# Kernel optimization log

Hardware: AMD Instinct MI355X
Metric: run time of the kernel (lower is better)

The kernel has to match this reference:

```python
import jax, jax.numpy as jnp
import numpy as np

B, T_ENC, T_DEC, D, H, O = 256, 512, 64, 64, 512, 512


def setup_inputs() -> dict:
    key = jax.random.key(0)
    ks = jax.random.split(key, 13)
    s = 1.0 / np.sqrt(H)  # PyTorch LSTM/Linear init scale
    u = lambda k, shape: jax.random.uniform(k, shape, jnp.float32, -s, s)
    return {
        "enc_inp": jax.random.normal(ks[0], (B, T_ENC, D), jnp.float32),
        "dec_inp": jax.random.normal(ks[1], (B, T_DEC, D), jnp.float32),
        "enc_Wih": u(ks[2], (4 * H, D)),
        "enc_Whh": u(ks[3], (4 * H, H)),
        "enc_bih": u(ks[4], (4 * H,)),
        "enc_bhh": u(ks[5], (4 * H,)),
        "dec_Wih": u(ks[6], (4 * H, D)),
        "dec_Whh": u(ks[7], (4 * H, H)),
        "dec_bih": u(ks[8], (4 * H,)),
        "dec_bhh": u(ks[9], (4 * H,)),
        "out_W": u(ks[10], (O, H)),
        "out_b": u(ks[11], (O,)),
    }


def _lstm_cell(h, c, x_t, Wih, Whh, bih, bhh):
    # PyTorch gate order: i, f, g, o
    z = x_t @ Wih.T + h @ Whh.T + (bih + bhh)  # [B, 4H]
    i, f, g, o = jnp.split(z, 4, axis=-1)
    c2 = jax.nn.sigmoid(f) * c + jax.nn.sigmoid(i) * jnp.tanh(g)
    h2 = jax.nn.sigmoid(o) * jnp.tanh(c2)
    return h2, c2


def reference(enc_inp, dec_inp, enc_Wih, enc_Whh, enc_bih, enc_bhh,
              dec_Wih, dec_Whh, dec_bih, dec_bhh, out_W, out_b):
    b = enc_inp.shape[0]
    h0 = jnp.zeros((b, H), enc_inp.dtype)
    c0 = jnp.zeros((b, H), enc_inp.dtype)

    # Encoder: single-layer LSTM over T_enc; only final (h, c) are used.
    def enc_step(carry, x_t):
        h, c = carry
        h2, c2 = _lstm_cell(h, c, x_t, enc_Wih, enc_Whh, enc_bih, enc_bhh)
        return (h2, c2), None

    (h, c), _ = jax.lax.scan(enc_step, (h0, c0), jnp.swapaxes(enc_inp, 0, 1))

    # Decoder: fused per-step LSTM + output projection over T_dec.
    def dec_step(carry, x_t):
        h, c = carry
        h2, c2 = _lstm_cell(h, c, x_t, dec_Wih, dec_Whh, dec_bih, dec_bhh)
        y = h2 @ out_W.T + out_b
        return (h2, c2), (y, h2)

    _, (ys, hs) = jax.lax.scan(dec_step, (h, c), jnp.swapaxes(dec_inp, 0, 1))

    dec_outputs = jnp.swapaxes(ys, 0, 1)  # [B, T_dec, O]
    dec_hiddens = jnp.swapaxes(hs, 0, 1)  # [B, T_dec, H]
    return dec_outputs, dec_hiddens
```

## Files before the change

### kernel.cpp

```cpp
#include <hip/hip_runtime.h>

typedef unsigned short ushort_t;
typedef unsigned long long u64;
typedef __attribute__((ext_vector_type(8))) __bf16 bf16x8;
typedef __attribute__((ext_vector_type(4))) float f32x4;

#define B 256
#define TENC 512
#define TDEC 64
#define DIN 64
#define HD 512
#define OD 512
#define GG 256
#define NGRP 16
#define KTOT 576
#define KI 18
#define NT 512

__device__ __forceinline__ float b2f(ushort_t v) {
  union { unsigned u; float f; } x; x.u = ((unsigned)v) << 16; return x.f;
}
__device__ __forceinline__ ushort_t f2b(float f) {
  union { float f; unsigned u; } x; x.f = f;
  unsigned r = x.u + 0x7fffu + ((x.u >> 16) & 1u);
  return (ushort_t)(r >> 16);
}
__device__ __forceinline__ float sigmf(float x) { return 1.f / (1.f + __expf(-x)); }
__device__ __forceinline__ float tanhf_fast(float x) {
  float e = __expf(2.f * x);
  return 1.f - 2.f / (e + 1.f);
}
__device__ __forceinline__ float ld_elem(const void* p, size_t i, bool f32) {
  return f32 ? ((const float*)p)[i] : b2f(((const ushort_t*)p)[i]);
}
__device__ __forceinline__ bf16x8 cvt8(const float* f) {
  f32x4 u = *(const f32x4*)f, v = *(const f32x4*)(f + 4);
  bf16x8 r;
  r[0] = (__bf16)u[0]; r[1] = (__bf16)u[1]; r[2] = (__bf16)u[2]; r[3] = (__bf16)u[3];
  r[4] = (__bf16)v[0]; r[5] = (__bf16)v[1]; r[6] = (__bf16)v[2]; r[7] = (__bf16)v[3];
  return r;
}
__device__ __forceinline__ bf16x8 ld_h16(const ushort_t* p) {
  union { u64 q[2]; bf16x8 v; } x;
  x.q[0] = __hip_atomic_load((const u64*)p,     __ATOMIC_RELAXED, __HIP_MEMORY_SCOPE_AGENT);
  x.q[1] = __hip_atomic_load((const u64*)p + 1, __ATOMIC_RELAXED, __HIP_MEMORY_SCOPE_AGENT);
  return x.v;
}

__global__ void detect(const ushort_t* w, unsigned* flag) {
  if (threadIdx.x == 0) {
    unsigned f = 0;
    for (int i = 0; i < 128; ++i) {
      float v = b2f(w[i]);
      if (!(v * v < 1.f)) f = 1;
    }
    *flag = f;
  }
}

__global__ __launch_bounds__(NT, 2) void lstm_seq(
    const void* enc_inp, const void* dec_inp,
    const void* eWih, const void* eWhh, const void* ebih, const void* ebhh,
    const void* dWih, const void* dWhh, const void* dbih, const void* dbhh,
    ushort_t* hbuf0, ushort_t* hbuf1,
    unsigned* flags,
    void* dout, const unsigned* mode)
{
  __shared__ __align__(16) char Hs[16384];
  __shared__ __align__(16) float Zs[8][16][20];
  __shared__ float Bias[128];

  const bool f32m = (*mode != 0);
  char* hid = (char*)dout + (size_t)B * TDEC * OD * (f32m ? 4 : 2);

  const int tid = threadIdx.x;
  const int lane = tid & 63;
  const int w = tid >> 6;
  const int wg = blockIdx.x;
  const int bg = wg & 15;
  const int ug = wg >> 4;
  const int fm = lane & 15;
  const int q = lane >> 4;
  const int row0 = bg * 16;
  const int u0w = ug * 32 + w * 4;

  const int crow = lane >> 2;
  const int cdu = lane & 3;
  float creg = 0.f;

  bf16x8 bfrag[KI];
  unsigned bstep = 0;

  for (int phase = 0; phase < 2; ++phase) {
    const void* Wih = phase ? dWih : eWih;
    const void* Whh = phase ? dWhh : eWhh;
    const void* bih = phase ? dbih : ebih;
    const void* bhh = phase ? dbhh : ebhh;
    const void* xin = phase ? dec_inp : enc_inp;
    const int T = phase ? TDEC : TENC;
    const int xstr = phase ? (TDEC * DIN) : (TENC * DIN);

    {
      const int grow = (fm >> 2) * HD + u0w + (fm & 3);
      for (int i = 0; i < KI; ++i) {
        union { ushort_t s[8]; bf16x8 v; } uf;
        const int k0 = i * 32 + q * 8;
#pragma unroll
        for (int e = 0; e < 8; ++e) {
          const int k = k0 + e;
          float wv = (k < HD) ? ld_elem(Whh, (size_t)grow * HD + k, f32m)
                              : ld_elem(Wih, (size_t)grow * DIN + (k - HD), f32m);
          uf.s[e] = f2b(wv);
        }
        bfrag[i] = uf.v;
      }
    }
    __syncthreads();
    if (tid < 128) {
      const int w_ = tid >> 4, n = tid & 15;
      const int grow = (n >> 2) * HD + ug * 32 + w_ * 4 + (n & 3);
      Bias[tid] = ld_elem(bih, grow, f32m) + ld_elem(bhh, grow, f32m);
    }
    __syncthreads();

    for (int t = 0; t < T; ++t) {
      const ushort_t* hcur = (bstep & 1) ? hbuf1 : hbuf0;
      ushort_t* hnxt = (bstep & 1) ? hbuf0 : hbuf1;

      f32x4 acca = {0.f, 0.f, 0.f, 0.f}, accb = {0.f, 0.f, 0.f, 0.f};
      if (!f32m) {
        const ushort_t* x0 = (const ushort_t*)xin + (size_t)(row0 + fm) * xstr + t * DIN;
        bf16x8 a0 = *(const bf16x8*)(x0 + q * 8);
        bf16x8 a1 = *(const bf16x8*)(x0 + 32 + q * 8);
        acca = __builtin_amdgcn_mfma_f32_16x16x32_bf16(a0, bfrag[16], acca, 0, 0, 0);
        accb = __builtin_amdgcn_mfma_f32_16x16x32_bf16(a1, bfrag[17], accb, 0, 0, 0);
      } else {
        const float* x0 = (const float*)xin + (size_t)(row0 + fm) * xstr + t * DIN;
        bf16x8 a0 = cvt8(x0 + q * 8);
        bf16x8 a1 = cvt8(x0 + 32 + q * 8);
        acca = __builtin_amdgcn_mfma_f32_16x16x32_bf16(a0, bfrag[16], acca, 0, 0, 0);
        accb = __builtin_amdgcn_mfma_f32_16x16x32_bf16(a1, bfrag[17], accb, 0, 0, 0);
      }

      if (bstep && tid < NGRP) {
        while (__hip_atomic_load(&flags[(bg + tid * 16) * 32],
                                 __ATOMIC_RELAXED, __HIP_MEMORY_SCOPE_AGENT) < bstep)
          __builtin_amdgcn_s_sleep(1);
      }
      __syncthreads();

#pragma unroll
      for (int j = 0; j < 2; ++j) {
        const int o = (j * NT + tid) * 16;
        const int ks = o >> 10;
        const int rem = o & 1023;
        const int r = rem >> 6;
        const int od = o ^ ((r & 7) << 4);
        *(bf16x8*)(Hs + od) =
            ld_h16(hcur + (size_t)ks * (B * 32) + (size_t)row0 * 32 + (rem >> 1));
      }
      __syncthreads();

      const int sw = (fm & 7) << 4;
#pragma unroll
      for (int i = 0; i < 16; i += 2) {
        bf16x8 a0 = *(const bf16x8*)(Hs + ((i * 1024 + fm * 64 + q * 16) ^ sw));
        bf16x8 a1 = *(const bf16x8*)(Hs + (((i + 1) * 1024 + fm * 64 + q * 16) ^ sw));
        acca = __builtin_amdgcn_mfma_f32_16x16x32_bf16(a0, bfrag[i],     acca, 0, 0, 0);
        accb = __builtin_amdgcn_mfma_f32_16x16x32_bf16(a1, bfrag[i + 1], accb, 0, 0, 0);
      }
      f32x4 acc = acca + accb;

#pragma unroll
      for (int r = 0; r < 4; ++r)
        Zs[w][q * 4 + r][fm] = acc[r];

      float h2;
      {
        const float* zr = Zs[w][crow];
        float zi = zr[cdu]      + Bias[w * 16 + cdu];
        float zf = zr[4 + cdu]  + Bias[w * 16 + 4 + cdu];
        float zg = zr[8 + cdu]  + Bias[w * 16 + 8 + cdu];
        float zo = zr[12 + cdu] + Bias[w * 16 + 12 + cdu];
        float c2 = sigmf(zf) * creg + sigmf(zi) * tanhf_fast(zg);
        h2 = sigmf(zo) * tanhf_fast(c2);
        creg = c2;
      }
      float hn = __shfl_xor(h2, 1);
      unsigned pk = (unsigned)f2b(h2) | ((unsigned)f2b(hn) << 16);
      if ((cdu & 1) == 0) {
        __hip_atomic_store((unsigned*)(hnxt + (size_t)ug * (B * 32)
                                       + (size_t)(row0 + crow) * 32 + w * 4 + cdu),
                           pk, __ATOMIC_RELAXED, __HIP_MEMORY_SCOPE_AGENT);
      }

      __syncthreads();
      if (tid == 0)
        __hip_atomic_store(&flags[wg * 32], bstep + 1,
                           __ATOMIC_RELAXED, __HIP_MEMORY_SCOPE_AGENT);

      if (phase && (cdu & 1) == 0) {
        size_t off = ((size_t)(row0 + crow) * TDEC + t) * HD + u0w + cdu;
        if (f32m) {
          float2 f2; f2.x = h2; f2.y = hn;
          *(float2*)((float*)hid + off) = f2;
        } else {
          *(unsigned*)((ushort_t*)hid + off) = pk;
        }
      }
      ++bstep;
    }
  }
}

__global__ __launch_bounds__(NT, 2) void out_proj(
    const void* Wo, const void* bo, void* dout, const unsigned* mode)
{
  __shared__ __align__(16) ushort_t Wc[16][520];
  const bool f32m = (*mode != 0);
  char* Ybase = (char*)dout;
  const char* Hd = Ybase + (size_t)B * TDEC * OD * (f32m ? 4 : 2);

  const int tid = threadIdx.x, lane = tid & 63, w = tid >> 6;
  const int fm = lane & 15, q = lane >> 4;
  const int nb = blockIdx.x & 31, mb = blockIdx.x >> 5;
  const int m0 = mb * 256, n0 = nb * 16;

  for (int idx = tid; idx < 16 * 512; idx += NT) {
    int n = idx >> 9, k = idx & 511;
    Wc[n][k] = f2b(ld_elem(Wo, (size_t)(n0 + n) * 512 + k, f32m));
  }
  __syncthreads();
  bf16x8 bfrag[16];
#pragma unroll
  for (int i = 0; i < 16; ++i) bfrag[i] = *(const bf16x8*)&Wc[fm][i * 32 + q * 8];

  f32x4 acc0 = {0.f, 0.f, 0.f, 0.f}, acc1 = {0.f, 0.f, 0.f, 0.f};
  if (!f32m) {
    const ushort_t* a0p = (const ushort_t*)Hd + (size_t)(m0 + w * 32 + fm) * 512;
    const ushort_t* a1p = (const ushort_t*)Hd + (size_t)(m0 + w * 32 + 16 + fm) * 512;
#pragma unroll
    for (int i = 0; i < 16; ++i) {
      int ko = i * 32 + q * 8;
      bf16x8 a0 = *(const bf16x8*)(a0p + ko);
      bf16x8 a1 = *(const bf16x8*)(a1p + ko);
      acc0 = __builtin_amdgcn_mfma_f32_16x16x32_bf16(a0, bfrag[i], acc0, 0, 0, 0);
      acc1 = __builtin_amdgcn_mfma_f32_16x16x32_bf16(a1, bfrag[i], acc1, 0, 0, 0);
    }
  } else {
    const float* a0p = (const float*)Hd + (size_t)(m0 + w * 32 + fm) * 512;
    const float* a1p = (const float*)Hd + (size_t)(m0 + w * 32 + 16 + fm) * 512;
#pragma unroll
    for (int i = 0; i < 16; ++i) {
      int ko = i * 32 + q * 8;
      bf16x8 a0 = cvt8(a0p + ko);
      bf16x8 a1 = cvt8(a1p + ko);
      acc0 = __builtin_amdgcn_mfma_f32_16x16x32_bf16(a0, bfrag[i], acc0, 0, 0, 0);
      acc1 = __builtin_amdgcn_mfma_f32_16x16x32_bf16(a1, bfrag[i], acc1, 0, 0, 0);
    }
  }
  float bias = ld_elem(bo, n0 + fm, f32m);
#pragma unroll
  for (int r = 0; r < 4; ++r) {
    size_t off0 = (size_t)(m0 + w * 32 + q * 4 + r) * 512 + n0 + fm;
    size_t off1 = off0 + (size_t)16 * 512;
    float v0 = acc0[r] + bias, v1 = acc1[r] + bias;
    if (f32m) { ((float*)Ybase)[off0] = v0; ((float*)Ybase)[off1] = v1; }
    else      { ((ushort_t*)Ybase)[off0] = f2b(v0); ((ushort_t*)Ybase)[off1] = f2b(v1); }
  }
}

extern "C" void kernel_launch(void* const* d_in, const int* in_sizes, int n_in,
                              void* d_out, int out_size, void* d_ws, size_t ws_size,
                              hipStream_t stream) {
  (void)in_sizes; (void)n_in; (void)out_size; (void)ws_size;
  const void* enc_inp = d_in[0];
  const void* dec_inp = d_in[1];
  const void* eWih = d_in[2];
  const void* eWhh = d_in[3];
  const void* ebih = d_in[4];
  const void* ebhh = d_in[5];
  const void* dWih = d_in[6];
  const void* dWhh = d_in[7];
  const void* dbih = d_in[8];
  const void* dbhh = d_in[9];
  const void* outW = d_in[10];
  const void* outb = d_in[11];

  unsigned* flag = (unsigned*)d_ws;

  char* ob = (char*)d_out;
  unsigned* flags = (unsigned*)(ob + 128);
  ushort_t* hbuf0 = (ushort_t*)(ob + 65536);
  ushort_t* hbuf1 = (ushort_t*)(ob + 65536 + (size_t)B * HD * 2);

  hipMemsetAsync(d_out, 0, 65536 + (size_t)B * HD * 2, stream);

  detect<<<1, 64, 0, stream>>>((const ushort_t*)eWhh, flag);
  lstm_seq<<<GG, NT, 0, stream>>>(enc_inp, dec_inp, eWih, eWhh, ebih, ebhh,
                                  dWih, dWhh, dbih, dbhh,
                                  hbuf0, hbuf1, flags, d_out, flag);
  out_proj<<<dim3(64 * 32), NT, 0, stream>>>(outW, outb, d_out, flag);
}
```

Baseline: 2.146 ms.

## Replace per-block step flags with tagged hidden-state slots for fine-grained sync

The persistent LSTM kernel drops its separate per-workgroup flag array and the spin-wait on it. Instead, each 32-bit packed hidden pair is stored together with a step tag in one 64-bit atomic slot, and consumers poll the slots until every needed tag matches the current step. This removes the barrier-then-flag-publish round trip and the flag polling latency from the serial recurrence critical path. In exchange the hidden-state buffers double in size, each load carries tag bytes, and the polling loop now retries many individual loads.

Measured after the change: 2.209 ms. 3.0% more time.

```diff
diff --git a/kernel.cpp b/kernel.cpp
--- a/kernel.cpp
+++ b/kernel.cpp
@@ -16,6 +16,7 @@
 #define KTOT 576
 #define KI 18
 #define NT 512
+#define SLOTQ (16 * 256 * 16)
 
 __device__ __forceinline__ float b2f(ushort_t v) {
   union { unsigned u; float f; } x; x.u = ((unsigned)v) << 16; return x.f;
@@ -40,12 +41,6 @@
   r[4] = (__bf16)v[0]; r[5] = (__bf16)v[1]; r[6] = (__bf16)v[2]; r[7] = (__bf16)v[3];
   return r;
 }
-__device__ __forceinline__ bf16x8 ld_h16(const ushort_t* p) {
-  union { u64 q[2]; bf16x8 v; } x;
-  x.q[0] = __hip_atomic_load((const u64*)p,     __ATOMIC_RELAXED, __HIP_MEMORY_SCOPE_AGENT);
-  x.q[1] = __hip_atomic_load((const u64*)p + 1, __ATOMIC_RELAXED, __HIP_MEMORY_SCOPE_AGENT);
-  return x.v;
-}
 
 __global__ void detect(const ushort_t* w, unsigned* flag) {
   if (threadIdx.x == 0) {
@@ -62,8 +57,7 @@
     const void* enc_inp, const void* dec_inp,
     const void* eWih, const void* eWhh, const void* ebih, const void* ebhh,
     const void* dWih, const void* dWhh, const void* dbih, const void* dbhh,
-    ushort_t* hbuf0, ushort_t* hbuf1,
-    unsigned* flags,
+    u64* slot0, u64* slot1,
     void* dout, const unsigned* mode)
 {
   __shared__ __align__(16) char Hs[16384];
@@ -88,6 +82,9 @@
   const int cdu = lane & 3;
   float creg = 0.f;
 
+  const size_t pidx = (size_t)ug * 4096 + (size_t)(row0 + crow) * 16
+                    + (size_t)(w * 2) + (cdu >> 1);
+
   bf16x8 bfrag[KI];
   unsigned bstep = 0;
 
@@ -124,8 +121,8 @@
     __syncthreads();
 
     for (int t = 0; t < T; ++t) {
-      const ushort_t* hcur = (bstep & 1) ? hbuf1 : hbuf0;
-      ushort_t* hnxt = (bstep & 1) ? hbuf0 : hbuf1;
+      const u64* sslot = (bstep & 1) ? slot1 : slot0;
+      u64* dslot = (bstep & 1) ? slot0 : slot1;
 
       f32x4 acca = {0.f, 0.f, 0.f, 0.f}, accb = {0.f, 0.f, 0.f, 0.f};
       if (!f32m) {
@@ -142,22 +139,30 @@
         accb = __builtin_amdgcn_mfma_f32_16x16x32_bf16(a1, bfrag[17], accb, 0, 0, 0);
       }
 
-      if (bstep && tid < NGRP) {
-        while (__hip_atomic_load(&flags[(bg + tid * 16) * 32],
-                                 __ATOMIC_RELAXED, __HIP_MEMORY_SCOPE_AGENT) < bstep)
-          __builtin_amdgcn_s_sleep(1);
-      }
       __syncthreads();
 
-#pragma unroll
-      for (int j = 0; j < 2; ++j) {
-        const int o = (j * NT + tid) * 16;
-        const int ks = o >> 10;
-        const int rem = o & 1023;
-        const int r = rem >> 6;
-        const int od = o ^ ((r & 7) << 4);
-        *(bf16x8*)(Hs + od) =
-            ld_h16(hcur + (size_t)ks * (B * 32) + (size_t)row0 * 32 + (rem >> 1));
+      {
+        const unsigned tag = bstep;
+        unsigned done = 0;
+        do {
+#pragma unroll
+          for (int j = 0; j < 4; ++j) {
+            if (done & (1u << j)) continue;
+            const int c = tid + (j << 9);
+            const int ugs = c >> 7, r = (c >> 3) & 15, pr = c & 7;
+            const u64* p = sslot + ((size_t)ugs * 4096
+                                    + (size_t)(row0 + r) * 16 + (pr << 1));
+            u64 a = __hip_atomic_load(p,     __ATOMIC_RELAXED, __HIP_MEMORY_SCOPE_AGENT);
+            u64 b = __hip_atomic_load(p + 1, __ATOMIC_RELAXED, __HIP_MEMORY_SCOPE_AGENT);
+            if ((unsigned)(a >> 32) == tag && (unsigned)(b >> 32) == tag) {
+              const int od = (ugs * 1024 + r * 64 + pr * 8) ^ ((r & 7) << 4);
+              uint2 v; v.x = (unsigned)a; v.y = (unsigned)b;
+              *(uint2*)(Hs + od) = v;
+              done |= 1u << j;
+            }
+          }
+          if (done != 15u) __builtin_amdgcn_s_sleep(1);
+        } while (done != 15u);
       }
       __syncthreads();
 
@@ -189,15 +194,10 @@
       float hn = __shfl_xor(h2, 1);
       unsigned pk = (unsigned)f2b(h2) | ((unsigned)f2b(hn) << 16);
       if ((cdu & 1) == 0) {
-        __hip_atomic_store((unsigned*)(hnxt + (size_t)ug * (B * 32)
-                                       + (size_t)(row0 + crow) * 32 + w * 4 + cdu),
-                           pk, __ATOMIC_RELAXED, __HIP_MEMORY_SCOPE_AGENT);
-      }
-
-      __syncthreads();
-      if (tid == 0)
-        __hip_atomic_store(&flags[wg * 32], bstep + 1,
+        u64 val = (u64)pk | ((u64)(bstep + 1) << 32);
+        __hip_atomic_store(dslot + pidx, val,
                            __ATOMIC_RELAXED, __HIP_MEMORY_SCOPE_AGENT);
+      }
 
       if (phase && (cdu & 1) == 0) {
         size_t off = ((size_t)(row0 + crow) * TDEC + t) * HD + u0w + cdu;
@@ -290,15 +290,14 @@
   unsigned* flag = (unsigned*)d_ws;
 
   char* ob = (char*)d_out;
-  unsigned* flags = (unsigned*)(ob + 128);
-  ushort_t* hbuf0 = (ushort_t*)(ob + 65536);
-  ushort_t* hbuf1 = (ushort_t*)(ob + 65536 + (size_t)B * HD * 2);
-
-  hipMemsetAsync(d_out, 0, 65536 + (size_t)B * HD * 2, stream);
+  u64* slot0 = (u64*)(ob + 65536);
+  u64* slot1 = (u64*)(ob + 65536 + (size_t)SLOTQ * 8);
+
+  hipMemsetAsync(d_out, 0, 65536 + 2 * (size_t)SLOTQ * 8, stream);
 
   detect<<<1, 64, 0, stream>>>((const ushort_t*)eWhh, flag);
   lstm_seq<<<GG, NT, 0, stream>>>(enc_inp, dec_inp, eWih, eWhh, ebih, ebhh,
                                   dWih, dWhh, dbih, dbhh,
-                                  hbuf0, hbuf1, flags, d_out, flag);
+                                  slot0, slot1, d_out, flag);
   out_proj<<<dim3(64 * 32), NT, 0, stream>>>(outW, outb, d_out, flag);
 }
```
